# Kernel optimization log

Measured on AMD Instinct MI355X. Metric: run time of the kernel, lower is better.

The kernel has to match this reference:

```python
import jax, jax.numpy as jnp
import numpy as np
from functools import partial

K = 10
ALPHA = 0.99
CUT_DIM = 768
N_ITERS = 20
EPS = 1e-8

def setup_inputs() -> dict:
    key = jax.random.key(0)
    k1, k2 = jax.random.split(key)
    N, D, C = 10000, 768, 1000
    features = jax.random.normal(k1, (N, D), dtype=jnp.float32)
    classification_weight = jax.random.normal(k2, (C, D), dtype=jnp.float32) * 0.02
    return {"features": features, "classification_weight": classification_weight}

def reference(features, classification_weight):
    N = features.shape[0]
    # --- kNN affinity graph on L2-normalized (truncated) features ---
    f = features[:, :CUT_DIM]
    f = f / (jnp.linalg.norm(f, axis=1, keepdims=True) + EPS)
    sims = f @ f.T                                   # [N, N] cosine similarity
    diag = jnp.arange(N)
    sims = sims.at[diag, diag].set(-jnp.inf)         # exclude self-edges
    vals, idx = jax.lax.top_k(sims, K)               # [N, K]
    vals = jnp.maximum(vals, 0.0) ** 3               # sharpen affinities
    W = jnp.zeros((N, N), dtype=features.dtype).at[diag[:, None], idx].set(vals)
    W = 0.5 * (W + W.T)                              # symmetrize
    # --- symmetric normalization S = D^-1/2 W D^-1/2 ---
    d_inv_sqrt = jax.lax.rsqrt(W.sum(axis=1) + EPS)  # [N]
    S = W * d_inv_sqrt[:, None] * d_inv_sqrt[None, :]
    # --- initial soft pseudo-labels from the classifier ---
    Y = jax.nn.softmax(features @ classification_weight.T, axis=-1)  # [N, C]
    # --- iterative diffusion: Z <- alpha*S@Z + (1-alpha)*Y ---
    def step(_, Z):
        return ALPHA * (S @ Z) + (1.0 - ALPHA) * Y
    Z = jax.lax.fori_loop(0, N_ITERS, step, Y)
    return Z
```

## Files before the change

### kernel.cpp

```cpp
#include <hip/hip_runtime.h>

#define N_ROWS 10000
#define DIM    768
#define NCLS   1000
#define KNB    10
#define NITER  20
#define EPSV   1e-8f
#define JSPLIT 16
#define NRT    79
#define NJT    79
#define NCT    8
#define MAXE   2048
#define STR    40

typedef __attribute__((ext_vector_type(8))) short s8b;
typedef __attribute__((ext_vector_type(4))) float f4;
typedef __attribute__((ext_vector_type(8))) unsigned short us8;
typedef __attribute__((ext_vector_type(4))) unsigned short us4;

__device__ __forceinline__ unsigned short f2bf(float x) {
    unsigned u = __float_as_uint(x);
    unsigned r = u + 0x7FFFu + ((u >> 16) & 1u);
    return (unsigned short)(r >> 16);
}
__device__ __forceinline__ float bf2f(unsigned short b) {
    return __uint_as_float(((unsigned)b) << 16);
}

__global__ __launch_bounds__(192) void rownorm2_k(const float* __restrict__ feat,
                                                  unsigned short* __restrict__ nfh,
                                                  unsigned short* __restrict__ nfl,
                                                  float* __restrict__ rnorm) {
    int row = blockIdx.x;
    int t = threadIdx.x;
    const float4* src = (const float4*)(feat + (size_t)row * DIM);
    float4 v = src[t];
    float ss = v.x*v.x + v.y*v.y + v.z*v.z + v.w*v.w;
#pragma unroll
    for (int m = 1; m < 64; m <<= 1) ss += __shfl_xor(ss, m, 64);
    __shared__ float red[3];
    if ((t & 63) == 0) red[t >> 6] = ss;
    __syncthreads();
    float nrm = sqrtf(red[0] + red[1] + red[2]) + EPSV;
    float inv = 1.0f / nrm;
    if (t == 0) rnorm[row] = nrm;
    float xs[4] = {v.x*inv, v.y*inv, v.z*inv, v.w*inv};
    us4 h, l;
#pragma unroll
    for (int j = 0; j < 4; ++j) {
        unsigned short hb = f2bf(xs[j]);
        h[j] = hb;
        l[j] = f2bf(xs[j] - bf2f(hb));
    }
    *(us4*)(nfh + (size_t)row * DIM + t*4) = h;
    *(us4*)(nfl + (size_t)row * DIM + t*4) = l;
}

__global__ void split_k(const float* __restrict__ src,
                        unsigned short* __restrict__ h,
                        unsigned short* __restrict__ l, int n4) {
    int i = blockIdx.x * blockDim.x + threadIdx.x;
    if (i >= n4) return;
    float4 v = ((const float4*)src)[i];
    float xs[4] = {v.x, v.y, v.z, v.w};
    us4 hh, ll;
#pragma unroll
    for (int j = 0; j < 4; ++j) {
        unsigned short hb = f2bf(xs[j]);
        hh[j] = hb;
        ll[j] = f2bf(xs[j] - bf2f(hb));
    }
    ((us4*)h)[i] = hh; ((us4*)l)[i] = ll;
}

__global__ __launch_bounds__(256, 2) void simtopk_k(const unsigned short* __restrict__ nfh,
                                                    const unsigned short* __restrict__ nfl,
                                                    float* __restrict__ pv,
                                                    int* __restrict__ pi_) {
    __shared__ __align__(16) unsigned short S[2][4][128 * STR];

    int tid = threadIdx.x;
    int l = tid & 63, w = tid >> 6;
    int g = l >> 4, c = l & 15;

    int id = blockIdx.x;
    int pos = id >> 3, x8 = id & 7;
    int bi = pos % NRT;
    int js = x8 + 8 * (pos / NRT);
    int m0 = bi * 128;

    float lv[2][10]; int li[2][10];
#pragma unroll
    for (int rf = 0; rf < 2; ++rf)
#pragma unroll
        for (int s = 0; s < 10; ++s) { lv[rf][s] = -1e30f; li[rf][s] = 0x7fffffff; }

    int srow = tid >> 1, skh = tid & 1;
    int agr = m0 + srow;
    bool aval = agr < N_ROWS;
    size_t abase = (size_t)agr * DIM + skh * 16;
    int lbase = srow * STR + skh * 16;

    us8 rah0, rah1, ral0, ral1, rbh0, rbh1, rbl0, rbl1;
    {
        size_t ao = abase;
        rah0 = aval ? *(const us8*)(nfh + ao)     : (us8)0;
        rah1 = aval ? *(const us8*)(nfh + ao + 8) : (us8)0;
        ral0 = aval ? *(const us8*)(nfl + ao)     : (us8)0;
        ral1 = aval ? *(const us8*)(nfl + ao + 8) : (us8)0;
        int bgr = js * 128 + srow;
        bool bval = bgr < N_ROWS;
        size_t bo = (size_t)bgr * DIM + skh * 16;
        rbh0 = bval ? *(const us8*)(nfh + bo)     : (us8)0;
        rbh1 = bval ? *(const us8*)(nfh + bo + 8) : (us8)0;
        rbl0 = bval ? *(const us8*)(nfl + bo)     : (us8)0;
        rbl1 = bval ? *(const us8*)(nfl + bo + 8) : (us8)0;
    }

    for (int jt = js; jt < NJT; jt += JSPLIT) {
        f4 acc[2][8];
#pragma unroll
        for (int rf = 0; rf < 2; ++rf)
#pragma unroll
            for (int cf = 0; cf < 8; ++cf) acc[rf][cf] = (f4)0.0f;

        for (int ch = 0; ch < DIM / 32; ++ch) {
            int p = ch & 1;
            *(us8*)(&S[p][0][lbase])     = rah0;  *(us8*)(&S[p][0][lbase + 8]) = rah1;
            *(us8*)(&S[p][1][lbase])     = ral0;  *(us8*)(&S[p][1][lbase + 8]) = ral1;
            *(us8*)(&S[p][2][lbase])     = rbh0;  *(us8*)(&S[p][2][lbase + 8]) = rbh1;
            *(us8*)(&S[p][3][lbase])     = rbl0;  *(us8*)(&S[p][3][lbase + 8]) = rbl1;
            __syncthreads();
            int nch = ch + 1, njt = jt;
            if (nch == DIM / 32) { nch = 0; njt = jt + JSPLIT; }
            if (njt < NJT) {
                size_t ao = abase + (size_t)nch * 32;
                rah0 = aval ? *(const us8*)(nfh + ao)     : (us8)0;
                rah1 = aval ? *(const us8*)(nfh + ao + 8) : (us8)0;
                ral0 = aval ? *(const us8*)(nfl + ao)     : (us8)0;
                ral1 = aval ? *(const us8*)(nfl + ao + 8) : (us8)0;
                int bgr = njt * 128 + srow;
                bool bval = bgr < N_ROWS;
                size_t bo = (size_t)bgr * DIM + skh * 16 + (size_t)nch * 32;
                rbh0 = bval ? *(const us8*)(nfh + bo)     : (us8)0;
                rbh1 = bval ? *(const us8*)(nfh + bo + 8) : (us8)0;
                rbl0 = bval ? *(const us8*)(nfl + bo)     : (us8)0;
                rbl1 = bval ? *(const us8*)(nfl + bo + 8) : (us8)0;
            }
            s8b ah0 = *(const s8b*)(&S[p][0][(w*32 +  0 + c) * STR + g*8]);
            s8b ah1 = *(const s8b*)(&S[p][0][(w*32 + 16 + c) * STR + g*8]);
            s8b al0 = *(const s8b*)(&S[p][1][(w*32 +  0 + c) * STR + g*8]);
            s8b al1 = *(const s8b*)(&S[p][1][(w*32 + 16 + c) * STR + g*8]);
#pragma unroll
            for (int cf = 0; cf < 8; ++cf) {
                s8b bh = *(const s8b*)(&S[p][2][(cf*16 + c) * STR + g*8]);
                s8b bl = *(const s8b*)(&S[p][3][(cf*16 + c) * STR + g*8]);
                acc[0][cf] = __builtin_amdgcn_mfma_f32_16x16x32_bf16(bh, ah0, acc[0][cf], 0, 0, 0);
                acc[0][cf] = __builtin_amdgcn_mfma_f32_16x16x32_bf16(bl, ah0, acc[0][cf], 0, 0, 0);
                acc[0][cf] = __builtin_amdgcn_mfma_f32_16x16x32_bf16(bh, al0, acc[0][cf], 0, 0, 0);
                acc[1][cf] = __builtin_amdgcn_mfma_f32_16x16x32_bf16(bh, ah1, acc[1][cf], 0, 0, 0);
                acc[1][cf] = __builtin_amdgcn_mfma_f32_16x16x32_bf16(bl, ah1, acc[1][cf], 0, 0, 0);
                acc[1][cf] = __builtin_amdgcn_mfma_f32_16x16x32_bf16(bh, al1, acc[1][cf], 0, 0, 0);
            }
        }
#pragma unroll
        for (int rf = 0; rf < 2; ++rf) {
            int row = m0 + w*32 + rf*16 + c;
#pragma unroll
            for (int cf = 0; cf < 8; ++cf) {
                f4 a = acc[rf][cf];
                int col0 = jt * 128 + cf*16 + g*4;
                float mx = fmaxf(fmaxf(a[0], a[1]), fmaxf(a[2], a[3]));
                if (mx > lv[rf][9]) {
#pragma unroll
                    for (int r = 0; r < 4; ++r) {
                        int col = col0 + r;
                        float val = a[r];
                        if (col < N_ROWS && col != row && val > lv[rf][9]) {
                            lv[rf][9] = val; li[rf][9] = col;
#pragma unroll
                            for (int u = 9; u > 0; --u) {
                                if (lv[rf][u] > lv[rf][u-1]) {
                                    float t2 = lv[rf][u]; lv[rf][u] = lv[rf][u-1]; lv[rf][u-1] = t2;
                                    int   t3 = li[rf][u]; li[rf][u] = li[rf][u-1]; li[rf][u-1] = t3;
                                }
                            }
                        }
                    }
                }
            }
        }
    }

#pragma unroll
    for (int rf = 0; rf < 2; ++rf) {
        int grow = m0 + w*32 + rf*16 + c;
#pragma unroll 1
        for (int sel = 0; sel < KNB; ++sel) {
            float cv = lv[rf][0]; int ci = li[rf][0];
            float bv = cv; int bi2 = ci;
            float ov = __shfl_xor(bv, 16, 64); int oi = __shfl_xor(bi2, 16, 64);
            if (ov > bv || (ov == bv && oi < bi2)) { bv = ov; bi2 = oi; }
            ov = __shfl_xor(bv, 32, 64); oi = __shfl_xor(bi2, 32, 64);
            if (ov > bv || (ov == bv && oi < bi2)) { bv = ov; bi2 = oi; }
            if (cv == bv && ci == bi2) {
#pragma unroll
                for (int s = 0; s < 9; ++s) { lv[rf][s] = lv[rf][s+1]; li[rf][s] = li[rf][s+1]; }
                lv[rf][9] = -1e30f; li[rf][9] = 0x7fffffff;
            }
            if (g == 0 && grow < N_ROWS) {
                size_t o = ((size_t)js * N_ROWS + grow) * KNB + sel;
                pv[o] = bv; pi_[o] = bi2;
            }
        }
    }
}

__global__ __launch_bounds__(256, 2) void gemm2_k(const unsigned short* __restrict__ nfh,
                                                  const unsigned short* __restrict__ nfl,
                                                  const unsigned short* __restrict__ cwh,
                                                  const unsigned short* __restrict__ cwl,
                                                  const float* __restrict__ rnorm,
                                                  float* __restrict__ logits) {
    __shared__ __align__(16) unsigned short S[2][4][128 * STR];
    int tid = threadIdx.x;
    int l = tid & 63, w = tid >> 6;
    int g = l >> 4, c = l & 15;
    int m0 = blockIdx.x * 128, n0 = blockIdx.y * 128;

    int srow = tid >> 1, skh = tid & 1;
    int agr = m0 + srow;
    bool aval = agr < N_ROWS;
    size_t abase = (size_t)agr * DIM + skh * 16;
    int bgr = n0 + srow;
    bool bval = bgr < NCLS;
    size_t bbase = (size_t)bgr * DIM + skh * 16;
    int lbase = srow * STR + skh * 16;

    us8 rah0, rah1, ral0, ral1, rbh0, rbh1, rbl0, rbl1;
    rah0 = aval ? *(const us8*)(nfh + abase)     : (us8)0;
    rah1 = aval ? *(const us8*)(nfh + abase + 8) : (us8)0;
    ral0 = aval ? *(const us8*)(nfl + abase)     : (us8)0;
    ral1 = aval ? *(const us8*)(nfl + abase + 8) : (us8)0;
    rbh0 = bval ? *(const us8*)(cwh + bbase)     : (us8)0;
    rbh1 = bval ? *(const us8*)(cwh + bbase + 8) : (us8)0;
    rbl0 = bval ? *(const us8*)(cwl + bbase)     : (us8)0;
    rbl1 = bval ? *(const us8*)(cwl + bbase + 8) : (us8)0;

    f4 acc[2][8];
#pragma unroll
    for (int rf = 0; rf < 2; ++rf)
#pragma unroll
        for (int cf = 0; cf < 8; ++cf) acc[rf][cf] = (f4)0.0f;

    for (int ch = 0; ch < DIM / 32; ++ch) {
        int p = ch & 1;
        *(us8*)(&S[p][0][lbase])     = rah0;  *(us8*)(&S[p][0][lbase + 8]) = rah1;
        *(us8*)(&S[p][1][lbase])     = ral0;  *(us8*)(&S[p][1][lbase + 8]) = ral1;
        *(us8*)(&S[p][2][lbase])     = rbh0;  *(us8*)(&S[p][2][lbase + 8]) = rbh1;
        *(us8*)(&S[p][3][lbase])     = rbl0;  *(us8*)(&S[p][3][lbase + 8]) = rbl1;
        __syncthreads();
        if (ch + 1 < DIM / 32) {
            size_t ao = abase + (size_t)(ch + 1) * 32;
            size_t bo = bbase + (size_t)(ch + 1) * 32;
            rah0 = aval ? *(const us8*)(nfh + ao)     : (us8)0;
            rah1 = aval ? *(const us8*)(nfh + ao + 8) : (us8)0;
            ral0 = aval ? *(const us8*)(nfl + ao)     : (us8)0;
            ral1 = aval ? *(const us8*)(nfl + ao + 8) : (us8)0;
            rbh0 = bval ? *(const us8*)(cwh + bo)     : (us8)0;
            rbh1 = bval ? *(const us8*)(cwh + bo + 8) : (us8)0;
            rbl0 = bval ? *(const us8*)(cwl + bo)     : (us8)0;
            rbl1 = bval ? *(const us8*)(cwl + bo + 8) : (us8)0;
        }
        s8b ah0 = *(const s8b*)(&S[p][0][(w*32 +  0 + c) * STR + g*8]);
        s8b ah1 = *(const s8b*)(&S[p][0][(w*32 + 16 + c) * STR + g*8]);
        s8b al0 = *(const s8b*)(&S[p][1][(w*32 +  0 + c) * STR + g*8]);
        s8b al1 = *(const s8b*)(&S[p][1][(w*32 + 16 + c) * STR + g*8]);
#pragma unroll
        for (int cf = 0; cf < 8; ++cf) {
            s8b bh = *(const s8b*)(&S[p][2][(cf*16 + c) * STR + g*8]);
            s8b bl = *(const s8b*)(&S[p][3][(cf*16 + c) * STR + g*8]);
            acc[0][cf] = __builtin_amdgcn_mfma_f32_16x16x32_bf16(bh, ah0, acc[0][cf], 0, 0, 0);
            acc[0][cf] = __builtin_amdgcn_mfma_f32_16x16x32_bf16(bl, ah0, acc[0][cf], 0, 0, 0);
            acc[0][cf] = __builtin_amdgcn_mfma_f32_16x16x32_bf16(bh, al0, acc[0][cf], 0, 0, 0);
            acc[1][cf] = __builtin_amdgcn_mfma_f32_16x16x32_bf16(bh, ah1, acc[1][cf], 0, 0, 0);
            acc[1][cf] = __builtin_amdgcn_mfma_f32_16x16x32_bf16(bl, ah1, acc[1][cf], 0, 0, 0);
            acc[1][cf] = __builtin_amdgcn_mfma_f32_16x16x32_bf16(bh, al1, acc[1][cf], 0, 0, 0);
        }
    }
#pragma unroll
    for (int rf = 0; rf < 2; ++rf) {
        int row = m0 + w*32 + rf*16 + c;
        if (row < N_ROWS) {
            float rn = rnorm[row];
#pragma unroll
            for (int cf = 0; cf < 8; ++cf) {
                f4 a = acc[rf][cf];
#pragma unroll
                for (int r = 0; r < 4; ++r) {
                    int col = n0 + cf*16 + g*4 + r;
                    if (col < NCLS) logits[(size_t)row * NCLS + col] = a[r] * rn;
                }
            }
        }
    }
}

__global__ __launch_bounds__(256) void softmax_k(const float* __restrict__ logits,
                                                 float* __restrict__ Y) {
    int row = blockIdx.x;
    const float* src = logits + (size_t)row * NCLS;
    __shared__ float sl[NCLS];
    __shared__ float red[4];
    int t = threadIdx.x;
    float mx = -1e30f;
    for (int cc = t; cc < NCLS; cc += 256) { float x = src[cc]; sl[cc] = x; mx = fmaxf(mx, x); }
#pragma unroll
    for (int m = 1; m < 64; m <<= 1) mx = fmaxf(mx, __shfl_xor(mx, m, 64));
    if ((t & 63) == 0) red[t >> 6] = mx;
    __syncthreads();
    mx = fmaxf(fmaxf(red[0], red[1]), fmaxf(red[2], red[3]));
    float sum = 0.f;
    for (int cc = t; cc < NCLS; cc += 256) { float e = expf(sl[cc] - mx); sl[cc] = e; sum += e; }
#pragma unroll
    for (int m = 1; m < 64; m <<= 1) sum += __shfl_xor(sum, m, 64);
    __syncthreads();
    if ((t & 63) == 0) red[t >> 6] = sum;
    __syncthreads();
    float inv = 1.0f / (red[0] + red[1] + red[2] + red[3]);
    float* dst = Y + (size_t)row * NCLS;
    for (int cc = t; cc < NCLS; cc += 256) dst[cc] = sl[cc] * inv;
}

__global__ void topmerge_k(float* __restrict__ pv, const int* __restrict__ pi_,
                           float* __restrict__ tv, int* __restrict__ ti_) {
    int row = blockIdx.x * blockDim.x + threadIdx.x;
    if (row >= N_ROWS) return;
    for (int sel = 0; sel < KNB; ++sel) {
        float best = -1e30f; long bslot = -1;
        for (int js = 0; js < JSPLIT; ++js) {
            size_t base = ((size_t)js * N_ROWS + row) * KNB;
            for (int k = 0; k < KNB; ++k) {
                float v = pv[base + k];
                if (v > best) { best = v; bslot = (long)(base + k); }
            }
        }
        tv[(size_t)row * KNB + sel] = best;
        ti_[(size_t)row * KNB + sel] = pi_[bslot];
        pv[bslot] = -1e30f;
    }
}

__global__ void edgecount_k(const float* __restrict__ tv, const int* __restrict__ ti_,
                            float* __restrict__ deg, int* __restrict__ cnt) {
    int e = blockIdx.x * blockDim.x + threadIdx.x;
    if (e >= N_ROWS * KNB) return;
    int i = e / KNB;
    int j = ti_[e];
    float v = fmaxf(tv[e], 0.f);
    float wv = 0.5f * v * v * v;
    atomicAdd(&deg[i], wv);
    atomicAdd(&deg[j], wv);
    atomicAdd(&cnt[i], 1);
    atomicAdd(&cnt[j], 1);
}

__global__ __launch_bounds__(1024) void scan_k(const int* __restrict__ cnt,
                                               int* __restrict__ rowptr,
                                               int* __restrict__ cur,
                                               const float* __restrict__ deg,
                                               float* __restrict__ dis) {
    __shared__ int sb[1024];
    int t = threadIdx.x;
    int carry = 0;
    for (int base = 0; base < N_ROWS; base += 1024) {
        int idx = base + t;
        int x = (idx < N_ROWS) ? cnt[idx] : 0;
        sb[t] = x;
        __syncthreads();
        for (int offc = 1; offc < 1024; offc <<= 1) {
            int add = (t >= offc) ? sb[t - offc] : 0;
            __syncthreads();
            sb[t] += add;
            __syncthreads();
        }
        int incl = sb[t];
        int tot = sb[1023];
        if (idx < N_ROWS) {
            rowptr[idx + 1] = carry + incl;
            cur[idx] = carry + incl - x;
            if (idx == 0) rowptr[0] = 0;
            dis[idx] = 1.0f / (sqrtf(deg[idx] + EPSV));
        }
        __syncthreads();
        carry += tot;
    }
}

__global__ void fill_k(const float* __restrict__ tv, const int* __restrict__ ti_,
                       const float* __restrict__ dis, int* __restrict__ cur,
                       int* __restrict__ cols, float* __restrict__ wts) {
    int e = blockIdx.x * blockDim.x + threadIdx.x;
    if (e >= N_ROWS * KNB) return;
    int i = e / KNB;
    int j = ti_[e];
    float v = fmaxf(tv[e], 0.f);
    float wv = 0.5f * v * v * v;
    float s = 0.99f * wv * dis[i] * dis[j];
    int p1 = atomicAdd(&cur[i], 1); cols[p1] = j; wts[p1] = s;
    int p2 = atomicAdd(&cur[j], 1); cols[p2] = i; wts[p2] = s;
}

__global__ __launch_bounds__(256) void spmv_k(const int* __restrict__ rowptr,
                                              const int* __restrict__ cols,
                                              const float* __restrict__ wts,
                                              const float* __restrict__ Zin,
                                              const float* __restrict__ Y,
                                              float* __restrict__ Zout) {
    int i = blockIdx.x;
    int b = rowptr[i], e = rowptr[i + 1];
    int nnz = e - b;
    __shared__ int   cs[MAXE];
    __shared__ float wsh[MAXE];
    int nl = min(nnz, MAXE);
    for (int t = threadIdx.x; t < nl; t += 256) { cs[t] = cols[b + t]; wsh[t] = wts[b + t]; }
    __syncthreads();
    const float beta = (float)(1.0 - 0.99);
    for (int cc = threadIdx.x; cc < NCLS; cc += 256) {
        float acc = beta * Y[(size_t)i * NCLS + cc];
        for (int k = 0; k < nl; ++k) acc += wsh[k] * Zin[(size_t)cs[k] * NCLS + cc];
        for (int k = MAXE; k < nnz; ++k) acc += wts[b + k] * Zin[(size_t)cols[b + k] * NCLS + cc];
        Zout[(size_t)i * NCLS + cc] = acc;
    }
}

extern "C" void kernel_launch(void* const* d_in, const int* in_sizes, int n_in,
                              void* d_out, int out_size, void* d_ws, size_t ws_size,
                              hipStream_t stream) {
    const float* feat = (const float*)d_in[0];
    const float* cw   = (const float*)d_in[1];
    float* out = (float*)d_out;
    char* ws = (char*)d_ws;
    size_t off = 0;
    auto alloc = [&](size_t b) { size_t o = off; off = (off + b + 255) & ~(size_t)255; return o; };
    unsigned short* nfh = (unsigned short*)(ws + alloc((size_t)N_ROWS * DIM * 2));
    unsigned short* nfl = (unsigned short*)(ws + alloc((size_t)N_ROWS * DIM * 2));
    unsigned short* cwh = (unsigned short*)(ws + alloc((size_t)NCLS * DIM * 2));
    unsigned short* cwl = (unsigned short*)(ws + alloc((size_t)NCLS * DIM * 2));
    float* rnorm = (float*)(ws + alloc(N_ROWS * 4));
    float* ZA   = (float*)(ws + alloc((size_t)N_ROWS * NCLS * 4));
    float* Y    = (float*)(ws + alloc((size_t)N_ROWS * NCLS * 4));
    float* pv   = (float*)(ws + alloc((size_t)JSPLIT * N_ROWS * KNB * 4));
    int*   pi_  = (int*)  (ws + alloc((size_t)JSPLIT * N_ROWS * KNB * 4));
    float* tv   = (float*)(ws + alloc((size_t)N_ROWS * KNB * 4));
    int*   ti_  = (int*)  (ws + alloc((size_t)N_ROWS * KNB * 4));
    float* deg  = (float*)(ws + alloc(N_ROWS * 4));
    int*   cnt  = (int*)  (ws + alloc(N_ROWS * 4));
    int*   rowptr = (int*)(ws + alloc((N_ROWS + 1) * 4));
    int*   cur  = (int*)  (ws + alloc(N_ROWS * 4));
    float* dis  = (float*)(ws + alloc(N_ROWS * 4));
    int*   cols = (int*)  (ws + alloc((size_t)2 * N_ROWS * KNB * 4));
    float* wts  = (float*)(ws + alloc((size_t)2 * N_ROWS * KNB * 4));
    if (off > ws_size) return;

    hipMemsetAsync(deg, 0, N_ROWS * 4, stream);
    hipMemsetAsync(cnt, 0, N_ROWS * 4, stream);

    rownorm2_k<<<N_ROWS, 192, 0, stream>>>(feat, nfh, nfl, rnorm);
    split_k<<<(NCLS * DIM / 4 + 255) / 256, 256, 0, stream>>>(cw, cwh, cwl, NCLS * DIM / 4);

    dim3 gl(NRT, NCT);
    gemm2_k<<<gl, 256, 0, stream>>>(nfh, nfl, cwh, cwl, rnorm, ZA);
    softmax_k<<<N_ROWS, 256, 0, stream>>>(ZA, Y);

    simtopk_k<<<NRT * JSPLIT, 256, 0, stream>>>(nfh, nfl, pv, pi_);
    topmerge_k<<<(N_ROWS + 255) / 256, 256, 0, stream>>>(pv, pi_, tv, ti_);

    edgecount_k<<<(N_ROWS * KNB + 255) / 256, 256, 0, stream>>>(tv, ti_, deg, cnt);
    scan_k<<<1, 1024, 0, stream>>>(cnt, rowptr, cur, deg, dis);
    fill_k<<<(N_ROWS * KNB + 255) / 256, 256, 0, stream>>>(tv, ti_, dis, cur, cols, wts);

    const float* zin = Y;
    for (int it = 0; it < NITER; ++it) {
        float* zout = (it & 1) ? out : ZA;
        spmv_k<<<N_ROWS, 256, 0, stream>>>(rowptr, cols, wts, zin, Y, zout);
        zin = zout;
    }
}
```

Before: 2.673 ms.

## Load A fragments directly to registers, swizzle B tile, vectorize SpMV

The similarity/top-k kernel no longer stages the A tile in shared memory. Each wave loads its own A fragments straight from global memory into registers, prefetched one chunk ahead. Only the B tile goes through LDS, laid out with an XOR swizzle instead of padded rows, which halves LDS traffic and footprint and cuts bank conflicts. The SpMV kernel now uses float4 loads with 250 active threads per row instead of scalar loads. The trade-off is uncoalesced 16-byte global reads for A and idle threads in the SpMV blocks.

```diff
diff --git a/kernel.cpp b/kernel.cpp
--- a/kernel.cpp
+++ b/kernel.cpp
@@ -77,7 +77,7 @@
                                                     const unsigned short* __restrict__ nfl,
                                                     float* __restrict__ pv,
                                                     int* __restrict__ pi_) {
-    __shared__ __align__(16) unsigned short S[2][4][128 * STR];
+    __shared__ __align__(16) unsigned short BS[2][2][128 * 32];
 
     int tid = threadIdx.x;
     int l = tid & 63, w = tid >> 6;
@@ -96,26 +96,32 @@
         for (int s = 0; s < 10; ++s) { lv[rf][s] = -1e30f; li[rf][s] = 0x7fffffff; }
 
     int srow = tid >> 1, skh = tid & 1;
-    int agr = m0 + srow;
-    bool aval = agr < N_ROWS;
-    size_t abase = (size_t)agr * DIM + skh * 16;
-    int lbase = srow * STR + skh * 16;
-
-    us8 rah0, rah1, ral0, ral1, rbh0, rbh1, rbl0, rbl1;
+    int sw = (srow >> 1) & 3;
+    int wb0 = srow * 32 + 8 * ((2 * skh)     ^ sw);
+    int wb1 = srow * 32 + 8 * ((2 * skh + 1) ^ sw);
+
+    int ar0 = m0 + w * 32 + c;
+    int ar1 = ar0 + 16;
+    bool av0 = ar0 < N_ROWS, av1 = ar1 < N_ROWS;
+    const size_t a0 = (size_t)ar0 * DIM + g * 8;
+    const size_t a1 = (size_t)ar1 * DIM + g * 8;
+
+    int rbo = c * 32 + 8 * (g ^ ((c >> 1) & 3));
+
+    us8 rbh0, rbh1, rbl0, rbl1;
     {
-        size_t ao = abase;
-        rah0 = aval ? *(const us8*)(nfh + ao)     : (us8)0;
-        rah1 = aval ? *(const us8*)(nfh + ao + 8) : (us8)0;
-        ral0 = aval ? *(const us8*)(nfl + ao)     : (us8)0;
-        ral1 = aval ? *(const us8*)(nfl + ao + 8) : (us8)0;
         int bgr = js * 128 + srow;
-        bool bval = bgr < N_ROWS;
-        size_t bo = (size_t)bgr * DIM + skh * 16;
-        rbh0 = bval ? *(const us8*)(nfh + bo)     : (us8)0;
-        rbh1 = bval ? *(const us8*)(nfh + bo + 8) : (us8)0;
-        rbl0 = bval ? *(const us8*)(nfl + bo)     : (us8)0;
-        rbl1 = bval ? *(const us8*)(nfl + bo + 8) : (us8)0;
-    }
+        bool bv = bgr < N_ROWS;
+        size_t bb = (size_t)bgr * DIM + skh * 16;
+        rbh0 = bv ? *(const us8*)(nfh + bb)     : (us8)0;
+        rbh1 = bv ? *(const us8*)(nfh + bb + 8) : (us8)0;
+        rbl0 = bv ? *(const us8*)(nfl + bb)     : (us8)0;
+        rbl1 = bv ? *(const us8*)(nfl + bb + 8) : (us8)0;
+    }
+    us8 cah0 = av0 ? *(const us8*)(nfh + a0) : (us8)0;
+    us8 cah1 = av1 ? *(const us8*)(nfh + a1) : (us8)0;
+    us8 cal0 = av0 ? *(const us8*)(nfl + a0) : (us8)0;
+    us8 cal1 = av1 ? *(const us8*)(nfl + a1) : (us8)0;
 
     for (int jt = js; jt < NJT; jt += JSPLIT) {
         f4 acc[2][8];
@@ -126,50 +132,48 @@
 
         for (int ch = 0; ch < DIM / 32; ++ch) {
             int p = ch & 1;
-            *(us8*)(&S[p][0][lbase])     = rah0;  *(us8*)(&S[p][0][lbase + 8]) = rah1;
-            *(us8*)(&S[p][1][lbase])     = ral0;  *(us8*)(&S[p][1][lbase + 8]) = ral1;
-            *(us8*)(&S[p][2][lbase])     = rbh0;  *(us8*)(&S[p][2][lbase + 8]) = rbh1;
-            *(us8*)(&S[p][3][lbase])     = rbl0;  *(us8*)(&S[p][3][lbase + 8]) = rbl1;
+            *(us8*)(&BS[p][0][wb0]) = rbh0;  *(us8*)(&BS[p][0][wb1]) = rbh1;
+            *(us8*)(&BS[p][1][wb0]) = rbl0;  *(us8*)(&BS[p][1][wb1]) = rbl1;
             __syncthreads();
+
             int nch = ch + 1, njt = jt;
             if (nch == DIM / 32) { nch = 0; njt = jt + JSPLIT; }
+            us8 nah0 = cah0, nah1 = cah1, nal0 = cal0, nal1 = cal1;
             if (njt < NJT) {
-                size_t ao = abase + (size_t)nch * 32;
-                rah0 = aval ? *(const us8*)(nfh + ao)     : (us8)0;
-                rah1 = aval ? *(const us8*)(nfh + ao + 8) : (us8)0;
-                ral0 = aval ? *(const us8*)(nfl + ao)     : (us8)0;
-                ral1 = aval ? *(const us8*)(nfl + ao + 8) : (us8)0;
-                int bgr = njt * 128 + srow;
-                bool bval = bgr < N_ROWS;
-                size_t bo = (size_t)bgr * DIM + skh * 16 + (size_t)nch * 32;
-                rbh0 = bval ? *(const us8*)(nfh + bo)     : (us8)0;
-                rbh1 = bval ? *(const us8*)(nfh + bo + 8) : (us8)0;
-                rbl0 = bval ? *(const us8*)(nfl + bo)     : (us8)0;
-                rbl1 = bval ? *(const us8*)(nfl + bo + 8) : (us8)0;
-            }
-            s8b ah0 = *(const s8b*)(&S[p][0][(w*32 +  0 + c) * STR + g*8]);
-            s8b ah1 = *(const s8b*)(&S[p][0][(w*32 + 16 + c) * STR + g*8]);
-            s8b al0 = *(const s8b*)(&S[p][1][(w*32 +  0 + c) * STR + g*8]);
-            s8b al1 = *(const s8b*)(&S[p][1][(w*32 + 16 + c) * STR + g*8]);
+                int nbgr = njt * 128 + srow;
+                bool nbv = nbgr < N_ROWS;
+                size_t nbb = (size_t)nbgr * DIM + skh * 16 + (size_t)nch * 32;
+                rbh0 = nbv ? *(const us8*)(nfh + nbb)     : (us8)0;
+                rbh1 = nbv ? *(const us8*)(nfh + nbb + 8) : (us8)0;
+                rbl0 = nbv ? *(const us8*)(nfl + nbb)     : (us8)0;
+                rbl1 = nbv ? *(const us8*)(nfl + nbb + 8) : (us8)0;
+                size_t ak = (size_t)nch * 32;
+                nah0 = av0 ? *(const us8*)(nfh + a0 + ak) : (us8)0;
+                nah1 = av1 ? *(const us8*)(nfh + a1 + ak) : (us8)0;
+                nal0 = av0 ? *(const us8*)(nfl + a0 + ak) : (us8)0;
+                nal1 = av1 ? *(const us8*)(nfl + a1 + ak) : (us8)0;
+            }
 #pragma unroll
             for (int cf = 0; cf < 8; ++cf) {
-                s8b bh = *(const s8b*)(&S[p][2][(cf*16 + c) * STR + g*8]);
-                s8b bl = *(const s8b*)(&S[p][3][(cf*16 + c) * STR + g*8]);
-                acc[0][cf] = __builtin_amdgcn_mfma_f32_16x16x32_bf16(bh, ah0, acc[0][cf], 0, 0, 0);
-                acc[0][cf] = __builtin_amdgcn_mfma_f32_16x16x32_bf16(bl, ah0, acc[0][cf], 0, 0, 0);
-                acc[0][cf] = __builtin_amdgcn_mfma_f32_16x16x32_bf16(bh, al0, acc[0][cf], 0, 0, 0);
-                acc[1][cf] = __builtin_amdgcn_mfma_f32_16x16x32_bf16(bh, ah1, acc[1][cf], 0, 0, 0);
-                acc[1][cf] = __builtin_amdgcn_mfma_f32_16x16x32_bf16(bl, ah1, acc[1][cf], 0, 0, 0);
-                acc[1][cf] = __builtin_amdgcn_mfma_f32_16x16x32_bf16(bh, al1, acc[1][cf], 0, 0, 0);
-            }
-        }
+                s8b bh = *(const s8b*)(&BS[p][0][rbo + cf * 512]);
+                s8b bl = *(const s8b*)(&BS[p][1][rbo + cf * 512]);
+                acc[0][cf] = __builtin_amdgcn_mfma_f32_16x16x32_bf16(bh, (s8b)cah0, acc[0][cf], 0, 0, 0);
+                acc[1][cf] = __builtin_amdgcn_mfma_f32_16x16x32_bf16(bh, (s8b)cah1, acc[1][cf], 0, 0, 0);
+                acc[0][cf] = __builtin_amdgcn_mfma_f32_16x16x32_bf16(bl, (s8b)cah0, acc[0][cf], 0, 0, 0);
+                acc[1][cf] = __builtin_amdgcn_mfma_f32_16x16x32_bf16(bl, (s8b)cah1, acc[1][cf], 0, 0, 0);
+                acc[0][cf] = __builtin_amdgcn_mfma_f32_16x16x32_bf16(bh, (s8b)cal0, acc[0][cf], 0, 0, 0);
+                acc[1][cf] = __builtin_amdgcn_mfma_f32_16x16x32_bf16(bh, (s8b)cal1, acc[1][cf], 0, 0, 0);
+            }
+            cah0 = nah0; cah1 = nah1; cal0 = nal0; cal1 = nal1;
+        }
+
 #pragma unroll
         for (int rf = 0; rf < 2; ++rf) {
-            int row = m0 + w*32 + rf*16 + c;
+            int row = m0 + w * 32 + rf * 16 + c;
 #pragma unroll
             for (int cf = 0; cf < 8; ++cf) {
                 f4 a = acc[rf][cf];
-                int col0 = jt * 128 + cf*16 + g*4;
+                int col0 = jt * 128 + cf * 16 + g * 4;
                 float mx = fmaxf(fmaxf(a[0], a[1]), fmaxf(a[2], a[3]));
                 if (mx > lv[rf][9]) {
 #pragma unroll
@@ -194,7 +198,7 @@
 
 #pragma unroll
     for (int rf = 0; rf < 2; ++rf) {
-        int grow = m0 + w*32 + rf*16 + c;
+        int grow = m0 + w * 32 + rf * 16 + c;
 #pragma unroll 1
         for (int sel = 0; sel < KNB; ++sel) {
             float cv = lv[rf][0]; int ci = li[rf][0];
@@ -425,12 +429,22 @@
     int nl = min(nnz, MAXE);
     for (int t = threadIdx.x; t < nl; t += 256) { cs[t] = cols[b + t]; wsh[t] = wts[b + t]; }
     __syncthreads();
-    const float beta = (float)(1.0 - 0.99);
-    for (int cc = threadIdx.x; cc < NCLS; cc += 256) {
-        float acc = beta * Y[(size_t)i * NCLS + cc];
-        for (int k = 0; k < nl; ++k) acc += wsh[k] * Zin[(size_t)cs[k] * NCLS + cc];
-        for (int k = MAXE; k < nnz; ++k) acc += wts[b + k] * Zin[(size_t)cols[b + k] * NCLS + cc];
-        Zout[(size_t)i * NCLS + cc] = acc;
+    int t = threadIdx.x;
+    if (t < NCLS / 4) {
+        const float beta = (float)(1.0 - 0.99);
+        float4 y = ((const float4*)(Y + (size_t)i * NCLS))[t];
+        float4 acc = make_float4(beta * y.x, beta * y.y, beta * y.z, beta * y.w);
+        for (int k = 0; k < nl; ++k) {
+            float wv = wsh[k];
+            float4 z = ((const float4*)(Zin + (size_t)cs[k] * NCLS))[t];
+            acc.x += wv * z.x; acc.y += wv * z.y; acc.z += wv * z.z; acc.w += wv * z.w;
+        }
+        for (int k = MAXE; k < nnz; ++k) {
+            float wv = wts[b + k];
+            float4 z = ((const float4*)(Zin + (size_t)cols[b + k] * NCLS))[t];
+            acc.x += wv * z.x; acc.y += wv * z.y; acc.z += wv * z.z; acc.w += wv * z.w;
+        }
+        ((float4*)(Zout + (size_t)i * NCLS))[t] = acc;
     }
 }
 
```

Result: slower. 2.982 ms (+11.6%).
